# Optimization experiments

Measured on AMD Instinct MI355X. Metric: run time of the kernel, lower is better.

## Reference

```python
import jax, jax.numpy as jnp
import numpy as np

GRID_SIZE = 128
FEATURE_SIZE = 16
HIDDEN_SIZE = 64
N_POINTS = 2097152


def setup_inputs() -> dict:
    key = jax.random.key(0)
    ks = jax.random.split(key, 8)
    points = jax.random.uniform(ks[0], (N_POINTS, 3), dtype=jnp.float32)
    grid = jax.random.normal(ks[1], (GRID_SIZE, GRID_SIZE, GRID_SIZE, FEATURE_SIZE), dtype=jnp.float32)
    # torch nn.Linear default init: U(-1/sqrt(fan_in), 1/sqrt(fan_in))
    def linear(k, fan_in, fan_out):
        kw, kb = jax.random.split(k)
        bound = 1.0 / np.sqrt(fan_in)
        W = jax.random.uniform(kw, (fan_out, fan_in), minval=-bound, maxval=bound, dtype=jnp.float32)
        b = jax.random.uniform(kb, (fan_out,), minval=-bound, maxval=bound, dtype=jnp.float32)
        return W, b
    W1, b1 = linear(ks[2], FEATURE_SIZE, HIDDEN_SIZE)
    W2, b2 = linear(ks[3], HIDDEN_SIZE, HIDDEN_SIZE)
    W3, b3 = linear(ks[4], HIDDEN_SIZE, 1)
    return {"points": points, "grid": grid, "W1": W1, "b1": b1,
            "W2": W2, "b2": b2, "W3": W3, "b3": b3}


def reference(points, grid, W1, b1, W2, b2, W3, b3):
    gs = grid.shape[0]
    # nearest-grid-node index: scale to [0, gs-1], clamp, round
    p = jnp.clip(points * (gs - 1), 0.0, gs - 1)
    idx = jnp.round(p).astype(jnp.int32)  # (N, 3)
    feats = grid[idx[:, 0], idx[:, 1], idx[:, 2]]  # (N, F) gather
    h = jax.nn.relu(feats @ W1.T + b1)
    h = jax.nn.relu(h @ W2.T + b2)
    occ = jnp.tanh(h @ W3.T + b3)  # (N, 1)
    return occ
```

## Files before the change

kernel.cpp:

```cpp
#include <hip/hip_runtime.h>
#include <hip/hip_fp16.h>
#include <cstdint>
#include <cstddef>


typedef _Float16 half8 __attribute__((ext_vector_type(8)));
typedef float float4v __attribute__((ext_vector_type(4)));
typedef __attribute__((address_space(3))) uint32_t lds_u32;
typedef __attribute__((address_space(1))) const uint32_t glb_u32;

#define WPB 4
#define G   4
#define NC  4

__device__ inline uint32_t pack_f16x2(float a, float b) {
    union { _Float16 h[2]; uint32_t u; } v;
    v.h[0] = (_Float16)a;
    v.h[1] = (_Float16)b;
    return v.u;
}

__global__ __launch_bounds__(256, 3) void occ_mlp_kernel(
    const float* __restrict__ pts,
    const float* __restrict__ grid,
    const float* __restrict__ W1, const float* __restrict__ b1,
    const float* __restrict__ W2, const float* __restrict__ b2,
    const float* __restrict__ W3, const float* __restrict__ b3,
    float* __restrict__ out, int nPoints)
{
    __shared__ float sbuf[WPB][2][G * 256];

    const int lane = threadIdx.x & 63;
    const int l15  = lane & 15;
    const int quad = lane >> 4;
    const int wib  = threadIdx.x >> 6;
    const int tile0 = (blockIdx.x * WPB + wib) * (G * NC);
    const int nTiles = (nPoints + 15) >> 4;
    if (tile0 >= nTiles) return;

    float* const buf0 = &sbuf[wib][0][0];
    float* const buf1 = &sbuf[wib][1][0];

    half8 A1[4];
#pragma unroll
    for (int t = 0; t < 4; ++t) {
        half8 f = {};
        if (quad < 2) {
            const float* row = W1 + (16 * t + l15) * 16 + quad * 8;
#pragma unroll
            for (int j = 0; j < 8; ++j) f[j] = (_Float16)row[j];
        } else if (quad == 2) {
            f[0] = (_Float16)b1[16 * t + l15];
        }
        A1[t] = f;
    }
    half8 A2[4][2];
#pragma unroll
    for (int t = 0; t < 4; ++t)
#pragma unroll
        for (int kk = 0; kk < 2; ++kk) {
            const float* row = W2 + (16 * t + l15) * 64 + 32 * kk + 8 * quad;
            half8 f;
#pragma unroll
            for (int j = 0; j < 8; ++j) f[j] = (_Float16)row[j];
            A2[t][kk] = f;
        }
    float4v bias2[4];
    float w3v[4][4];
#pragma unroll
    for (int t = 0; t < 4; ++t)
#pragma unroll
        for (int r = 0; r < 4; ++r) {
            int h = 16 * t + 4 * quad + r;
            bias2[t][r] = b2[h];
            w3v[t][r]   = W3[h];
        }
    const float bias3 = b3[0];

    const int src0 = l15 + 16 * ((2 * quad) & 3);
    const int src1 = l15 + 16 * ((2 * quad + 1) & 3);
    const bool sel = (quad >> 1) != 0;

    const int gpt  = lane >> 2;
    const int gseg = lane & 3;
    const int maxP = nPoints - 1;

    float Rx[G], Ry[G], Rz[G];

    auto loadChunkPts = [&](int c) {
#pragma unroll
        for (int u = 0; u < G; ++u) {
            int p = (tile0 + c * G + u) * 16 + gpt;
            p = p > maxP ? maxP : p;
            const float* q = pts + 3 * p;
            Rx[u] = q[0]; Ry[u] = q[1]; Rz[u] = q[2];
        }
    };
    auto dmaChunk = [&](float* buf) {
#pragma unroll
        for (int u = 0; u < G; ++u) {
            const int ix = (int)rintf(fminf(fmaxf(Rx[u] * 127.0f, 0.0f), 127.0f));
            const int iy = (int)rintf(fminf(fmaxf(Ry[u] * 127.0f, 0.0f), 127.0f));
            const int iz = (int)rintf(fminf(fmaxf(Rz[u] * 127.0f, 0.0f), 127.0f));
            const int ofs = ((((ix << 7) | iy) << 7) | iz) << 4;
            const float* ga = grid + ofs + (gseg << 2);
            __builtin_amdgcn_global_load_lds((glb_u32*)ga,
                                             (lds_u32*)(buf + u * 256), 16, 0, 0);
        }
    };

    loadChunkPts(0);
    dmaChunk(buf0);
    loadChunkPts(1);

#pragma unroll
    for (int k = 0; k < NC; ++k) {
        float* const bufC = (k & 1) ? buf1 : buf0;
        float* const bufN = (k & 1) ? buf0 : buf1;

        asm volatile("s_waitcnt vmcnt(0)" ::: "memory");

        if (k + 1 < NC) dmaChunk(bufN);
        if (k + 2 < NC) loadChunkPts(k + 2);

        float o[G];
#pragma unroll
        for (int u = 0; u < G; ++u) {
            half8 bfrag = {};
            if (quad < 2) {
                const float4* gp = reinterpret_cast<const float4*>(
                    bufC + u * 256 + (l15 << 4) + (quad << 3));
                const float4 f0 = gp[0];
                const float4 f1 = gp[1];
                bfrag[0] = (_Float16)f0.x; bfrag[1] = (_Float16)f0.y;
                bfrag[2] = (_Float16)f0.z; bfrag[3] = (_Float16)f0.w;
                bfrag[4] = (_Float16)f1.x; bfrag[5] = (_Float16)f1.y;
                bfrag[6] = (_Float16)f1.z; bfrag[7] = (_Float16)f1.w;
            } else if (quad == 2) {
                bfrag[0] = (_Float16)1.0f;
            }

            float4v C1[4];
#pragma unroll
            for (int t = 0; t < 4; ++t) {
                float4v zacc = {};
                C1[t] = __builtin_amdgcn_mfma_f32_16x16x32_f16(A1[t], bfrag, zacc, 0, 0, 0);
            }

            uint32_t P[4][2];
#pragma unroll
            for (int t = 0; t < 4; ++t) {
                P[t][0] = pack_f16x2(fmaxf(C1[t][0], 0.0f), fmaxf(C1[t][1], 0.0f));
                P[t][1] = pack_f16x2(fmaxf(C1[t][2], 0.0f), fmaxf(C1[t][3], 0.0f));
            }

            union Frag { uint32_t u[4]; half8 h; } B2[2];
#pragma unroll
            for (int kk = 0; kk < 2; ++kk) {
                const uint32_t x0a = (uint32_t)__shfl((int)P[2 * kk    ][0], src0);
                const uint32_t x0b = (uint32_t)__shfl((int)P[2 * kk + 1][0], src0);
                const uint32_t x1a = (uint32_t)__shfl((int)P[2 * kk    ][1], src0);
                const uint32_t x1b = (uint32_t)__shfl((int)P[2 * kk + 1][1], src0);
                const uint32_t y0a = (uint32_t)__shfl((int)P[2 * kk    ][0], src1);
                const uint32_t y0b = (uint32_t)__shfl((int)P[2 * kk + 1][0], src1);
                const uint32_t y1a = (uint32_t)__shfl((int)P[2 * kk    ][1], src1);
                const uint32_t y1b = (uint32_t)__shfl((int)P[2 * kk + 1][1], src1);
                B2[kk].u[0] = sel ? x0b : x0a;
                B2[kk].u[1] = sel ? x1b : x1a;
                B2[kk].u[2] = sel ? y0b : y0a;
                B2[kk].u[3] = sel ? y1b : y1a;
            }

            float4v C2[4];
#pragma unroll
            for (int t = 0; t < 4; ++t) C2[t] = bias2[t];
#pragma unroll
            for (int kk = 0; kk < 2; ++kk)
#pragma unroll
                for (int t = 0; t < 4; ++t)
                    C2[t] = __builtin_amdgcn_mfma_f32_16x16x32_f16(A2[t][kk], B2[kk].h, C2[t], 0, 0, 0);

            float z = 0.0f;
#pragma unroll
            for (int t = 0; t < 4; ++t)
#pragma unroll
                for (int r = 0; r < 4; ++r)
                    z = fmaf(fmaxf(C2[t][r], 0.0f), w3v[t][r], z);
            z += __shfl_xor(z, 16);
            z += __shfl_xor(z, 32);
            const float e = __expf(2.0f * (z + bias3));
            o[u] = fmaf(-2.0f, __builtin_amdgcn_rcpf(e + 1.0f), 1.0f);
        }

        const float osel = (quad == 0) ? o[0] : (quad == 1) ? o[1]
                         : (quad == 2) ? o[2] : o[3];
        const int pstore = (tile0 + k * G) * 16 + lane;
        if (pstore <= maxP) out[pstore] = osel;
    }
}

extern "C" void kernel_launch(void* const* d_in, const int* in_sizes, int n_in,
                              void* d_out, int out_size, void* d_ws, size_t ws_size,
                              hipStream_t stream)
{
    const float* pts  = (const float*)d_in[0];
    const float* grid = (const float*)d_in[1];
    const float* W1   = (const float*)d_in[2];
    const float* b1   = (const float*)d_in[3];
    const float* W2   = (const float*)d_in[4];
    const float* b2   = (const float*)d_in[5];
    const float* W3   = (const float*)d_in[6];
    const float* b3   = (const float*)d_in[7];
    float* out = (float*)d_out;
    const int nPoints = in_sizes[0] / 3;

    const int nTiles = (nPoints + 15) >> 4;
    const int tilesPerBlock = WPB * G * NC;
    const int nBlocks = (nTiles + tilesPerBlock - 1) / tilesPerBlock;

    occ_mlp_kernel<<<dim3(nBlocks), dim3(256), 0, stream>>>(
        pts, grid, W1, b1, W2, b2, W3, b3, out, nPoints);
}
```

Measured before the change: 256.5 us.

## Replace LDS async gather with direct register feature loads and software pipelining

Removes the shared-memory staging buffers and global_load_lds DMA. Each lane now loads its own grid feature row straight into registers as two float4 loads, with a per-tile pipeline that prefetches points four tiles ahead and features two tiles ahead. The occupancy hint rises from 3 to 4 blocks because LDS is no longer used. The cost is more register pressure and reliance on compiler-inserted waitcnts instead of explicit chunk barriers.

```diff
diff --git a/kernel.cpp b/kernel.cpp
--- a/kernel.cpp
+++ b/kernel.cpp
@@ -6,12 +6,9 @@
 
 typedef _Float16 half8 __attribute__((ext_vector_type(8)));
 typedef float float4v __attribute__((ext_vector_type(4)));
-typedef __attribute__((address_space(3))) uint32_t lds_u32;
-typedef __attribute__((address_space(1))) const uint32_t glb_u32;
 
 #define WPB 4
-#define G   4
-#define NC  4
+#define NT  16
 
 __device__ inline uint32_t pack_f16x2(float a, float b) {
     union { _Float16 h[2]; uint32_t u; } v;
@@ -20,7 +17,7 @@
     return v.u;
 }
 
-__global__ __launch_bounds__(256, 3) void occ_mlp_kernel(
+__global__ __launch_bounds__(256, 4) void occ_mlp_kernel(
     const float* __restrict__ pts,
     const float* __restrict__ grid,
     const float* __restrict__ W1, const float* __restrict__ b1,
@@ -28,18 +25,14 @@
     const float* __restrict__ W3, const float* __restrict__ b3,
     float* __restrict__ out, int nPoints)
 {
-    __shared__ float sbuf[WPB][2][G * 256];
-
     const int lane = threadIdx.x & 63;
     const int l15  = lane & 15;
     const int quad = lane >> 4;
     const int wib  = threadIdx.x >> 6;
-    const int tile0 = (blockIdx.x * WPB + wib) * (G * NC);
+    const int tile0 = (blockIdx.x * WPB + wib) * NT;
     const int nTiles = (nPoints + 15) >> 4;
     if (tile0 >= nTiles) return;
-
-    float* const buf0 = &sbuf[wib][0][0];
-    float* const buf1 = &sbuf[wib][1][0];
+    const int maxP = nPoints - 1;
 
     half8 A1[4];
 #pragma unroll
@@ -81,121 +74,109 @@
     const int src1 = l15 + 16 * ((2 * quad + 1) & 3);
     const bool sel = (quad >> 1) != 0;
 
-    const int gpt  = lane >> 2;
-    const int gseg = lane & 3;
-    const int maxP = nPoints - 1;
-
-    float Rx[G], Ry[G], Rz[G];
-
-    auto loadChunkPts = [&](int c) {
-#pragma unroll
-        for (int u = 0; u < G; ++u) {
-            int p = (tile0 + c * G + u) * 16 + gpt;
-            p = p > maxP ? maxP : p;
-            const float* q = pts + 3 * p;
-            Rx[u] = q[0]; Ry[u] = q[1]; Rz[u] = q[2];
-        }
+    float Px[4], Py[4], Pz[4];
+    float4 Fa[2], Fb[2];
+
+    auto loadPts = [&](int slot, int u) {
+        int p = (tile0 + u) * 16 + l15;
+        p = p > maxP ? maxP : p;
+        const float* q = pts + 3 * p;
+        Px[slot] = q[0]; Py[slot] = q[1]; Pz[slot] = q[2];
     };
-    auto dmaChunk = [&](float* buf) {
-#pragma unroll
-        for (int u = 0; u < G; ++u) {
-            const int ix = (int)rintf(fminf(fmaxf(Rx[u] * 127.0f, 0.0f), 127.0f));
-            const int iy = (int)rintf(fminf(fmaxf(Ry[u] * 127.0f, 0.0f), 127.0f));
-            const int iz = (int)rintf(fminf(fmaxf(Rz[u] * 127.0f, 0.0f), 127.0f));
+    auto loadFeat = [&](int fslot, int pslot) {
+        if (quad < 2) {
+            const int ix = (int)rintf(fminf(fmaxf(Px[pslot] * 127.0f, 0.0f), 127.0f));
+            const int iy = (int)rintf(fminf(fmaxf(Py[pslot] * 127.0f, 0.0f), 127.0f));
+            const int iz = (int)rintf(fminf(fmaxf(Pz[pslot] * 127.0f, 0.0f), 127.0f));
             const int ofs = ((((ix << 7) | iy) << 7) | iz) << 4;
-            const float* ga = grid + ofs + (gseg << 2);
-            __builtin_amdgcn_global_load_lds((glb_u32*)ga,
-                                             (lds_u32*)(buf + u * 256), 16, 0, 0);
+            const float4* g = reinterpret_cast<const float4*>(grid + ofs + (quad << 3));
+            Fa[fslot] = g[0];
+            Fb[fslot] = g[1];
         }
     };
 
-    loadChunkPts(0);
-    dmaChunk(buf0);
-    loadChunkPts(1);
-
-#pragma unroll
-    for (int k = 0; k < NC; ++k) {
-        float* const bufC = (k & 1) ? buf1 : buf0;
-        float* const bufN = (k & 1) ? buf0 : buf1;
-
-        asm volatile("s_waitcnt vmcnt(0)" ::: "memory");
-
-        if (k + 1 < NC) dmaChunk(bufN);
-        if (k + 2 < NC) loadChunkPts(k + 2);
-
-        float o[G];
-#pragma unroll
-        for (int u = 0; u < G; ++u) {
-            half8 bfrag = {};
-            if (quad < 2) {
-                const float4* gp = reinterpret_cast<const float4*>(
-                    bufC + u * 256 + (l15 << 4) + (quad << 3));
-                const float4 f0 = gp[0];
-                const float4 f1 = gp[1];
-                bfrag[0] = (_Float16)f0.x; bfrag[1] = (_Float16)f0.y;
-                bfrag[2] = (_Float16)f0.z; bfrag[3] = (_Float16)f0.w;
-                bfrag[4] = (_Float16)f1.x; bfrag[5] = (_Float16)f1.y;
-                bfrag[6] = (_Float16)f1.z; bfrag[7] = (_Float16)f1.w;
-            } else if (quad == 2) {
-                bfrag[0] = (_Float16)1.0f;
-            }
-
-            float4v C1[4];
-#pragma unroll
-            for (int t = 0; t < 4; ++t) {
-                float4v zacc = {};
-                C1[t] = __builtin_amdgcn_mfma_f32_16x16x32_f16(A1[t], bfrag, zacc, 0, 0, 0);
-            }
-
-            uint32_t P[4][2];
-#pragma unroll
-            for (int t = 0; t < 4; ++t) {
-                P[t][0] = pack_f16x2(fmaxf(C1[t][0], 0.0f), fmaxf(C1[t][1], 0.0f));
-                P[t][1] = pack_f16x2(fmaxf(C1[t][2], 0.0f), fmaxf(C1[t][3], 0.0f));
-            }
-
-            union Frag { uint32_t u[4]; half8 h; } B2[2];
-#pragma unroll
-            for (int kk = 0; kk < 2; ++kk) {
-                const uint32_t x0a = (uint32_t)__shfl((int)P[2 * kk    ][0], src0);
-                const uint32_t x0b = (uint32_t)__shfl((int)P[2 * kk + 1][0], src0);
-                const uint32_t x1a = (uint32_t)__shfl((int)P[2 * kk    ][1], src0);
-                const uint32_t x1b = (uint32_t)__shfl((int)P[2 * kk + 1][1], src0);
-                const uint32_t y0a = (uint32_t)__shfl((int)P[2 * kk    ][0], src1);
-                const uint32_t y0b = (uint32_t)__shfl((int)P[2 * kk + 1][0], src1);
-                const uint32_t y1a = (uint32_t)__shfl((int)P[2 * kk    ][1], src1);
-                const uint32_t y1b = (uint32_t)__shfl((int)P[2 * kk + 1][1], src1);
-                B2[kk].u[0] = sel ? x0b : x0a;
-                B2[kk].u[1] = sel ? x1b : x1a;
-                B2[kk].u[2] = sel ? y0b : y0a;
-                B2[kk].u[3] = sel ? y1b : y1a;
-            }
-
-            float4v C2[4];
-#pragma unroll
-            for (int t = 0; t < 4; ++t) C2[t] = bias2[t];
-#pragma unroll
-            for (int kk = 0; kk < 2; ++kk)
-#pragma unroll
-                for (int t = 0; t < 4; ++t)
-                    C2[t] = __builtin_amdgcn_mfma_f32_16x16x32_f16(A2[t][kk], B2[kk].h, C2[t], 0, 0, 0);
-
-            float z = 0.0f;
+    loadPts(0, 0); loadPts(1, 1); loadPts(2, 2); loadPts(3, 3);
+    loadFeat(0, 0);
+    loadFeat(1, 1);
+
+    float o[4];
+
+#pragma unroll
+    for (int u = 0; u < NT; ++u) {
+        half8 bfrag = {};
+        if (quad < 2) {
+            const float4 f0 = Fa[u & 1];
+            const float4 f1 = Fb[u & 1];
+            bfrag[0] = (_Float16)f0.x; bfrag[1] = (_Float16)f0.y;
+            bfrag[2] = (_Float16)f0.z; bfrag[3] = (_Float16)f0.w;
+            bfrag[4] = (_Float16)f1.x; bfrag[5] = (_Float16)f1.y;
+            bfrag[6] = (_Float16)f1.z; bfrag[7] = (_Float16)f1.w;
+        } else if (quad == 2) {
+            bfrag[0] = (_Float16)1.0f;
+        }
+
+        if (u + 4 < NT) loadPts(u & 3, u + 4);
+        if (u + 2 < NT) loadFeat(u & 1, (u + 2) & 3);
+
+        float4v C1[4];
+#pragma unroll
+        for (int t = 0; t < 4; ++t) {
+            float4v zacc = {};
+            C1[t] = __builtin_amdgcn_mfma_f32_16x16x32_f16(A1[t], bfrag, zacc, 0, 0, 0);
+        }
+
+        uint32_t P[4][2];
+#pragma unroll
+        for (int t = 0; t < 4; ++t) {
+            P[t][0] = pack_f16x2(fmaxf(C1[t][0], 0.0f), fmaxf(C1[t][1], 0.0f));
+            P[t][1] = pack_f16x2(fmaxf(C1[t][2], 0.0f), fmaxf(C1[t][3], 0.0f));
+        }
+
+        union Frag { uint32_t u[4]; half8 h; } B2[2];
+#pragma unroll
+        for (int kk = 0; kk < 2; ++kk) {
+            const uint32_t x0a = (uint32_t)__shfl((int)P[2 * kk    ][0], src0);
+            const uint32_t x0b = (uint32_t)__shfl((int)P[2 * kk + 1][0], src0);
+            const uint32_t x1a = (uint32_t)__shfl((int)P[2 * kk    ][1], src0);
+            const uint32_t x1b = (uint32_t)__shfl((int)P[2 * kk + 1][1], src0);
+            const uint32_t y0a = (uint32_t)__shfl((int)P[2 * kk    ][0], src1);
+            const uint32_t y0b = (uint32_t)__shfl((int)P[2 * kk + 1][0], src1);
+            const uint32_t y1a = (uint32_t)__shfl((int)P[2 * kk    ][1], src1);
+            const uint32_t y1b = (uint32_t)__shfl((int)P[2 * kk + 1][1], src1);
+            B2[kk].u[0] = sel ? x0b : x0a;
+            B2[kk].u[1] = sel ? x1b : x1a;
+            B2[kk].u[2] = sel ? y0b : y0a;
+            B2[kk].u[3] = sel ? y1b : y1a;
+        }
+
+        float4v C2[4];
+#pragma unroll
+        for (int t = 0; t < 4; ++t) C2[t] = bias2[t];
+#pragma unroll
+        for (int kk = 0; kk < 2; ++kk)
 #pragma unroll
             for (int t = 0; t < 4; ++t)
-#pragma unroll
-                for (int r = 0; r < 4; ++r)
-                    z = fmaf(fmaxf(C2[t][r], 0.0f), w3v[t][r], z);
-            z += __shfl_xor(z, 16);
-            z += __shfl_xor(z, 32);
-            const float e = __expf(2.0f * (z + bias3));
-            o[u] = fmaf(-2.0f, __builtin_amdgcn_rcpf(e + 1.0f), 1.0f);
-        }
-
-        const float osel = (quad == 0) ? o[0] : (quad == 1) ? o[1]
-                         : (quad == 2) ? o[2] : o[3];
-        const int pstore = (tile0 + k * G) * 16 + lane;
-        if (pstore <= maxP) out[pstore] = osel;
+                C2[t] = __builtin_amdgcn_mfma_f32_16x16x32_f16(A2[t][kk], B2[kk].h, C2[t], 0, 0, 0);
+
+        float z = 0.0f;
+#pragma unroll
+        for (int t = 0; t < 4; ++t)
+#pragma unroll
+            for (int r = 0; r < 4; ++r)
+                z = fmaf(fmaxf(C2[t][r], 0.0f), w3v[t][r], z);
+        z += __shfl_xor(z, 16);
+        z += __shfl_xor(z, 32);
+        const float e = __expf(2.0f * (z + bias3));
+        o[u & 3] = fmaf(-2.0f, __builtin_amdgcn_rcpf(e + 1.0f), 1.0f);
+
+        if ((u & 3) == 3) {
+            const float osel = (quad == 0) ? o[0] : (quad == 1) ? o[1]
+                             : (quad == 2) ? o[2] : o[3];
+            const int pstore = (tile0 + (u & ~3)) * 16 + lane;
+            if (pstore <= maxP) out[pstore] = osel;
+        }
+
+        asm volatile("" ::: "memory");
     }
 }
 
@@ -215,7 +196,7 @@
     const int nPoints = in_sizes[0] / 3;
 
     const int nTiles = (nPoints + 15) >> 4;
-    const int tilesPerBlock = WPB * G * NC;
+    const int tilesPerBlock = WPB * NT;
     const int nBlocks = (nTiles + tilesPerBlock - 1) / tilesPerBlock;
 
     occ_mlp_kernel<<<dim3(nBlocks), dim3(256), 0, stream>>>(
```

After: 360.9 us. 1.41x slower.
